# Kernel optimization log

Measured on AMD Instinct MI355X. Metric: run time of the kernel, lower is better.

## Reference

```python
import jax, jax.numpy as jnp
import numpy as np
import math

NUM_CLASSES = 80
CENTER_RADIUS = 2.5
EPS = 1e-7
IMG = 1280.0


def _ciou(gt, pd):
    # gt: [G,4] xyxy, pd: [A,4] xyxy -> CIoU [G,A] (matches ultralytics bbox_iou, CIoU=True)
    b1 = gt[:, None, :]
    b2 = pd[None, :, :]
    iw = jnp.clip(jnp.minimum(b1[..., 2], b2[..., 2]) - jnp.maximum(b1[..., 0], b2[..., 0]), 0.0)
    ih = jnp.clip(jnp.minimum(b1[..., 3], b2[..., 3]) - jnp.maximum(b1[..., 1], b2[..., 1]), 0.0)
    inter = iw * ih
    w1 = b1[..., 2] - b1[..., 0]; h1 = b1[..., 3] - b1[..., 1]
    w2 = b2[..., 2] - b2[..., 0]; h2 = b2[..., 3] - b2[..., 1]
    union = w1 * h1 + w2 * h2 - inter + EPS
    iou = inter / union
    cw = jnp.maximum(b1[..., 2], b2[..., 2]) - jnp.minimum(b1[..., 0], b2[..., 0])
    ch = jnp.maximum(b1[..., 3], b2[..., 3]) - jnp.minimum(b1[..., 1], b2[..., 1])
    c2 = cw * cw + ch * ch + EPS
    rho2 = ((b2[..., 0] + b2[..., 2] - b1[..., 0] - b1[..., 2]) ** 2 +
            (b2[..., 1] + b2[..., 3] - b1[..., 1] - b1[..., 3]) ** 2) / 4.0
    v = (4.0 / math.pi ** 2) * (jnp.arctan(w2 / (h2 + EPS)) - jnp.arctan(w1 / (h1 + EPS))) ** 2
    alpha = v / (v - iou + (1.0 + EPS))
    return iou - (rho2 / c2 + v * alpha)


def _assign_one(scores, boxes, gt_lab, gt_box, valid, stride, anc):
    # scores [A,C], boxes [A,4], gt_lab [G], gt_box [G,4], valid [G] bool, stride [A,1], anc [A,2]
    G = gt_lab.shape[0]
    C = scores.shape[-1]
    # geometry constraint: anchor center within radius*stride of gt center
    gcx = (gt_box[:, 0] + gt_box[:, 2]) / 2.0
    gcy = (gt_box[:, 1] + gt_box[:, 3]) / 2.0
    cd = (stride[:, 0] * CENTER_RADIUS)[None, :]            # [1,A]
    in_center = (jnp.abs(anc[None, :, 0] - gcx[:, None]) < cd) & \
                (jnp.abs(anc[None, :, 1] - gcy[:, None]) < cd)
    in_center = in_center & valid[:, None]                  # [G,A]
    anchor_filter = in_center.any(axis=0)                   # [A]
    # pairwise CIoU (zeroed outside the filtered anchor set / invalid gts)
    ious = jnp.clip(_ciou(gt_box, boxes), 0.0)
    ious = ious * anchor_filter[None, :].astype(ious.dtype) * valid[:, None].astype(ious.dtype)
    iou_loss = -jnp.log(ious + 1e-8)
    # BCE(sqrt(p), onehot) summed over classes, computed without [G,A,C] tensor:
    # sum_c BCE = -sum_c log(1-p_c) - log p_{c_g} + log(1-p_{c_g})
    p = jnp.sqrt(scores)
    logp = jnp.clip(jnp.log(p), -100.0)
    log1mp = jnp.clip(jnp.log1p(-p), -100.0)
    base = -log1mp.sum(-1)                                  # [A]
    lp_g = jnp.take(logp, gt_lab, axis=1).T                 # [G,A]
    l1m_g = jnp.take(log1mp, gt_lab, axis=1).T              # [G,A]
    cls_loss = base[None, :] - lp_g + l1m_g
    # cost; extra 1e8/1e9 penalties emulate torch's exclusion of unfiltered anchors / invalid gts
    cost = (cls_loss + 3.0 * iou_loss
            + 1e6 * (~in_center).astype(cls_loss.dtype)
            + 1e8 * (~anchor_filter)[None, :].astype(cls_loss.dtype)
            + 1e9 * (~valid)[:, None].astype(cls_loss.dtype))
    # dynamic-k: sum of top-10 ious per gt
    topk_ious = jax.lax.top_k(ious, 10)[0]
    dyn_k = jnp.maximum((topk_ious.sum(-1) + 0.5).astype(jnp.int32), 1)
    # per-gt pick dyn_k lowest-cost anchors via rank
    ranks = jnp.argsort(jnp.argsort(cost, axis=-1), axis=-1)
    matching = (ranks < dyn_k[:, None]) & valid[:, None]    # [G,A] bool
    # conflict resolution: anchors matched to >1 gt keep min-cost gt
    cnt = matching.sum(0)                                   # [A]
    best_g = jnp.argmin(cost, axis=0)                       # [A]
    onehot_g = jnp.arange(G)[:, None] == best_g[None, :]
    matching = jnp.where(cnt[None, :] > 1, onehot_g, matching)
    fg = matching.any(axis=0)                               # [A]
    mg = jnp.argmax(matching, axis=0)                       # [A]
    pred_iou = (matching.astype(ious.dtype) * ious).sum(0)  # [A]
    labels = jnp.where(fg, gt_lab[mg], NUM_CLASSES).astype(jnp.int32)
    tboxes = gt_box[mg] * fg[:, None].astype(gt_box.dtype)
    tscores = jax.nn.one_hot(gt_lab[mg], C, dtype=scores.dtype) * (pred_iou * fg)[:, None]
    tgt_idx = jnp.where(fg, mg, 0).astype(jnp.int32)
    return labels, tboxes, tscores, fg, tgt_idx


def setup_inputs() -> dict:
    key = jax.random.key(0)
    ks = jax.random.split(key, 10)
    bs, A, G, C = 16, 33600, 64, NUM_CLASSES
    pd_scores = jax.random.uniform(ks[0], (bs, A, C), jnp.float32, 1e-4, 0.99)
    cxy = jax.random.uniform(ks[1], (bs, A, 2), jnp.float32, 0.0, IMG)
    wh = jax.random.uniform(ks[2], (bs, A, 2), jnp.float32, 8.0, 128.0)
    pd_bboxes = jnp.concatenate([cxy - wh / 2, cxy + wh / 2], axis=-1)
    anc_points = jax.random.uniform(ks[3], (A, 2), jnp.float32, 0.0, IMG)
    gt_labels = jax.random.randint(ks[4], (bs, G, 1), 0, C, jnp.int32)
    gcxy = jax.random.uniform(ks[5], (bs, G, 2), jnp.float32, 64.0, IMG - 64.0)
    gwh = jax.random.uniform(ks[6], (bs, G, 2), jnp.float32, 16.0, 256.0)
    gt_bboxes = jnp.concatenate([gcxy - gwh / 2, gcxy + gwh / 2], axis=-1)
    mask_gt = (jax.random.randint(ks[7], (bs, G, 1), 0, 5, jnp.int32) < 4).astype(jnp.int32)
    stride = (8.0 * (2.0 ** jax.random.randint(ks[8], (bs, A, 1), 0, 3, jnp.int32).astype(jnp.float32)))
    return {"pd_scores": pd_scores, "pd_bboxes": pd_bboxes, "anc_points": anc_points,
            "gt_labels": gt_labels, "gt_bboxes": gt_bboxes, "mask_gt": mask_gt, "stride": stride}


def reference(pd_scores, pd_bboxes, anc_points, gt_labels, gt_bboxes, mask_gt, stride):
    gt_lab = gt_labels[..., 0].astype(jnp.int32)
    valid = mask_gt[..., 0].astype(bool)
    fn = jax.vmap(_assign_one, in_axes=(0, 0, 0, 0, 0, 0, None))
    return fn(pd_scores, pd_bboxes, gt_lab, gt_bboxes, valid, stride, anc_points)
```

## Files before the change

### kernel.cpp

```cpp
#include <hip/hip_runtime.h>
#include <float.h>
#include <math.h>

#define NA 33600
#define NG 64
#define NC 80
#define NB 16
#define CRAD 2.5f
#define MCAP 12288

typedef float vfloat4 __attribute__((ext_vector_type(4)));

#define O_CNT   0ULL
#define O_AG    2150400ULL
#define O_AIOU  4300800ULL
#define O_BASE  6451200ULL
#define O_CCNT  8601600ULL
#define O_CONFC 8601664ULL
#define O_CONFL 8601728ULL
#define O_CA    8667264ULL
#define O_CBASE 9453696ULL
#define O_COLT  10240128ULL
#define WS_NEED_COLT (10240128ULL + 62914560ULL)
#define O_CPB   73154688ULL
#define O_CAP   76300416ULL
#define WS_NEED_PC (76300416ULL + 3145728ULL)
#define O_PIOU  79446144ULL
#define O_PCST  79528064ULL
#define O_PIDX  79609984ULL
#define O_PCI   79691904ULL
#define WS_NEED_SPLIT 79773824ULL

#define OFF_LAB 0L
#define OFF_TB  537600L
#define OFF_TS  2688000L
#define OFF_FG  45696000L
#define OFF_TGT 46233600L
#define OUT_TOTAL 46771200L

__device__ __forceinline__ float ciou_clip(float gx1, float gy1, float gx2, float gy2,
                                           float w1, float h1, float at1, float at2v,
                                           float4 pb) {
    float iw = fmaxf(fminf(gx2, pb.z) - fmaxf(gx1, pb.x), 0.f);
    float ih = fmaxf(fminf(gy2, pb.w) - fmaxf(gy1, pb.y), 0.f);
    float inter = iw * ih;
    float w2 = pb.z - pb.x, h2 = pb.w - pb.y;
    float uni = w1 * h1 + w2 * h2 - inter + 1e-7f;
    float iou = inter / uni;
    float cw = fmaxf(gx2, pb.z) - fminf(gx1, pb.x);
    float ch = fmaxf(gy2, pb.w) - fminf(gy1, pb.y);
    float c2 = cw * cw + ch * ch + 1e-7f;
    float dx = pb.x + pb.z - gx1 - gx2;
    float dy = pb.y + pb.w - gy1 - gy2;
    float rho2 = (dx * dx + dy * dy) * 0.25f;
    float dat = at2v - at1;
    float v = 0.4052847345693511f * (dat * dat);
    float alpha = v / ((v - iou) + 1.0000001f);
    float ci = iou - (rho2 / c2 + v * alpha);
    return fmaxf(ci, 0.f);
}

__global__ __launch_bounds__(256) void k1a_cand(
    const float* __restrict__ anc, const float* __restrict__ gbox,
    const int* __restrict__ gmask, const float* __restrict__ strd,
    int* __restrict__ candA, int* __restrict__ candCnt, int* __restrict__ cnt)
{
    __shared__ float s_gcx[NG], s_gcy[NG];
    __shared__ int s_val[NG];
    const int b = blockIdx.y, tid = threadIdx.x;
    if (tid < NG) {
        const float4 gb = ((const float4*)gbox)[b * NG + tid];
        s_gcx[tid] = (gb.x + gb.z) * 0.5f;
        s_gcy[tid] = (gb.y + gb.w) * 0.5f;
        s_val[tid] = gmask[b * NG + tid];
    }
    __syncthreads();
    const int a = blockIdx.x * 256 + tid;
    int f = 0;
    if (a < NA) {
        cnt[(long)b * NA + a] = 0;
        float2 ap = ((const float2*)anc)[a];
        float cd = strd[(long)b * NA + a] * CRAD;
        for (int g = 0; g < NG; ++g)
            if (s_val[g] && fabsf(ap.x - s_gcx[g]) < cd && fabsf(ap.y - s_gcy[g]) < cd) { f = 1; break; }
    }
    unsigned long long m = __ballot(f);
    int lane = tid & 63;
    int wcnt = __popcll(m);
    int pre = __popcll(m & ((1ULL << lane) - 1ULL));
    int base0 = 0;
    if (lane == 0 && wcnt) base0 = atomicAdd(&candCnt[b], wcnt);
    base0 = __shfl(base0, 0, 64);
    if (f) {
        int pos = base0 + pre;
        if (pos < MCAP) candA[b * MCAP + pos] = a;
    }
}

__global__ __launch_bounds__(256) void k1b_gather(
    const float* __restrict__ scores, const float* __restrict__ pdb,
    const float* __restrict__ anc, const float* __restrict__ strd,
    const int* __restrict__ candCnt, const int* __restrict__ candA,
    float* __restrict__ base, float* __restrict__ candBase,
    float* __restrict__ colT, int use_colT,
    float4* __restrict__ candPB, float4* __restrict__ candAp, int use_pc)
{
    __shared__ float s_l1m[64][81];
    const int b = blockIdx.y;
    int M = candCnt[b]; if (M > MCAP) M = MCAP;
    if (blockIdx.x * 64 >= M) return;
    const int q   = threadIdx.x >> 2;
    const int sub = threadIdx.x & 3;
    const int j = blockIdx.x * 64 + q;
    const bool active = (j < M);
    int a = 0;
    if (active) a = candA[b * MCAP + j];
    const long ia = (long)b * NA + a;
    if (active) {
        if (sub == 1 && use_pc) {
            float4 pb = ((const float4*)pdb)[ia];
            float2 ap = ((const float2*)anc)[a];
            float cd = strd[ia] * CRAD;
            float at2v = atanf((pb.z - pb.x) / ((pb.w - pb.y) + 1e-7f));
            candPB[b * MCAP + j] = pb;
            candAp[b * MCAP + j] = make_float4(ap.x, ap.y, cd, at2v);
        }
        const vfloat4* srow = (const vfloat4*)(scores + ia * NC);
        float* ct = colT + (long)b * NC * MCAP + j;
        #pragma unroll
        for (int qq = 0; qq < 5; ++qq) {
            vfloat4 s4 = __builtin_nontemporal_load(&srow[sub * 5 + qq]);
            float sv[4] = {s4.x, s4.y, s4.z, s4.w};
            #pragma unroll
            for (int k = 0; k < 4; ++k) {
                const int c = sub * 20 + 4 * qq + k;
                float p = sqrtf(sv[k]);
                float l1m = fmaxf(log1pf(-p), -100.f);
                s_l1m[q][c] = l1m;
                if (use_colT) {
                    float lp = fmaxf(logf(p), -100.f);
                    __builtin_nontemporal_store(l1m - lp, &ct[(long)c * MCAP]);
                }
            }
        }
    }
    __syncthreads();
    if (active && sub == 0) {
        float bsum = 0.f;
        #pragma unroll
        for (int c = 0; c < NC; ++c)
            bsum += s_l1m[q][c];
        const float bval = -bsum;
        base[ia] = bval;
        candBase[b * MCAP + j] = bval;
    }
}

__global__ __launch_bounds__(256) void k2_scan(
    const int* __restrict__ glab, const float* __restrict__ gbox,
    const int* __restrict__ gmask,
    const int* __restrict__ candCnt, const int* __restrict__ candA,
    const float* __restrict__ candBase, const float* __restrict__ colT,
    const float4* __restrict__ candPB, const float4* __restrict__ candAp,
    float* __restrict__ partIou, float* __restrict__ partCost,
    int* __restrict__ partIdx, float* __restrict__ partCi)
{
    const int i = blockIdx.y;
    const int s = blockIdx.x;
    const int b = (i & 7) | ((i >> 9) << 3);
    const int g = (i >> 3) & 63;
    if (gmask[b * NG + g] == 0) return;
    const int tid = threadIdx.x, lane = tid & 63, wid = tid >> 6;
    __shared__ float s_v[4];
    __shared__ int s_i[4];

    const float4 gb = ((const float4*)gbox)[b * NG + g];
    const int lab = glab[b * NG + g];
    const float gcx = (gb.x + gb.z) * 0.5f, gcy = (gb.y + gb.w) * 0.5f;
    const float w1 = gb.z - gb.x, h1 = gb.w - gb.y;
    const float at1 = atanf(w1 / (h1 + 1e-7f));
    const int bM = b * MCAP;
    int M = candCnt[b]; if (M > MCAP) M = MCAP;
    const float* colrow = colT + (long)(b * NC + lab) * MCAP;

    float liou[10]; int liodx[10];
    float lcost[10]; int lidx[10]; float lci[10];
    #pragma unroll
    for (int j = 0; j < 10; ++j) {
        liou[j] = 0.f;  liodx[j] = 0x40000000 + tid * 10 + j;
        lcost[j] = FLT_MAX; lidx[j] = 0x40000000 + tid * 10 + j; lci[j] = 0.f;
    }

    for (int jj = s * 256 + tid; jj < M; jj += 512) {
        const int a = candA[bM + jj];
        float4 pb = candPB[bM + jj];
        float4 t  = candAp[bM + jj];
        float ci = ciou_clip(gb.x, gb.y, gb.z, gb.w, w1, h1, at1, t.w, pb);
        bool inc = (fabsf(t.x - gcx) < t.z) && (fabsf(t.y - gcy) < t.z);
        float colv = candBase[bM + jj] + colrow[jj];
        float cost = colv + 3.0f * (-logf(ci + 1e-8f));
        if (!inc) cost += 1e6f;

        if (ci > 0.f && (ci > liou[9] || (ci == liou[9] && a < liodx[9]))) {
            int p10 = 0;
            #pragma unroll
            for (int k = 0; k < 10; ++k)
                p10 += (liou[k] > ci || (liou[k] == ci && liodx[k] < a)) ? 1 : 0;
            #pragma unroll
            for (int j = 9; j >= 0; --j) {
                float pv = (j > 0) ? liou[j - 1] : 0.f;
                int pvi  = (j > 0) ? liodx[j - 1] : 0;
                bool sh = (j > p10), he = (j == p10);
                liou[j]  = sh ? pv  : (he ? ci : liou[j]);
                liodx[j] = sh ? pvi : (he ? a  : liodx[j]);
            }
        }
        if (cost < lcost[9] || (cost == lcost[9] && a < lidx[9])) {
            int p10 = 0;
            #pragma unroll
            for (int k = 0; k < 10; ++k)
                p10 += (lcost[k] < cost || (lcost[k] == cost && lidx[k] < a)) ? 1 : 0;
            #pragma unroll
            for (int j = 9; j >= 0; --j) {
                float pv = (j > 0) ? lcost[j - 1] : FLT_MAX;
                int pvi  = (j > 0) ? lidx[j - 1] : 0;
                float pvc = (j > 0) ? lci[j - 1] : 0.f;
                bool sh = (j > p10), he = (j == p10);
                lcost[j] = sh ? pv  : (he ? cost : lcost[j]);
                lidx[j]  = sh ? pvi : (he ? a    : lidx[j]);
                lci[j]   = sh ? pvc : (he ? ci   : lci[j]);
            }
        }
    }

    const int pbase = i * 20 + s * 10;
    for (int it = 0; it < 10; ++it) {
        float bv = -2.f; int bi = 0x7fffffff;
        #pragma unroll
        for (int j = 0; j < 10; ++j)
            if (liou[j] > bv || (liou[j] == bv && liodx[j] < bi)) { bv = liou[j]; bi = liodx[j]; }
        for (int off = 32; off > 0; off >>= 1) {
            float ov = __shfl_down(bv, off, 64);
            int   oi = __shfl_down(bi, off, 64);
            if (ov > bv || (ov == bv && oi < bi)) { bv = ov; bi = oi; }
        }
        if (lane == 0) { s_v[wid] = bv; s_i[wid] = bi; }
        __syncthreads();
        float wv = s_v[0]; int wi = s_i[0];
        #pragma unroll
        for (int w = 1; w < 4; ++w)
            if (s_v[w] > wv || (s_v[w] == wv && s_i[w] < wi)) { wv = s_v[w]; wi = s_i[w]; }
        if (tid == 0) partIou[pbase + it] = wv;
        #pragma unroll
        for (int j = 0; j < 10; ++j)
            if (liou[j] == wv && liodx[j] == wi) { liou[j] = -2.f; liodx[j] = 0x7fffffff; }
        __syncthreads();
    }
    for (int it = 0; it < 10; ++it) {
        float bc = FLT_MAX; int bi = 0x7fffffff;
        #pragma unroll
        for (int j = 0; j < 10; ++j)
            if (lcost[j] < bc || (lcost[j] == bc && lidx[j] < bi)) { bc = lcost[j]; bi = lidx[j]; }
        for (int off = 32; off > 0; off >>= 1) {
            float oc = __shfl_down(bc, off, 64);
            int   oi = __shfl_down(bi, off, 64);
            if (oc < bc || (oc == bc && oi < bi)) { bc = oc; bi = oi; }
        }
        if (lane == 0) { s_v[wid] = bc; s_i[wid] = bi; }
        __syncthreads();
        float wc = s_v[0]; int wi = s_i[0];
        #pragma unroll
        for (int w = 1; w < 4; ++w)
            if (s_v[w] < wc || (s_v[w] == wc && s_i[w] < wi)) { wc = s_v[w]; wi = s_i[w]; }
        #pragma unroll
        for (int j = 0; j < 10; ++j)
            if (lcost[j] == wc && lidx[j] == wi) {
                partCost[pbase + it] = wc;
                partIdx[pbase + it]  = wi;
                partCi[pbase + it]   = lci[j];
                lcost[j] = FLT_MAX; lidx[j] = 0x7fffffff;
            }
        __syncthreads();
    }
}

__global__ __launch_bounds__(256) void k2b_merge(
    const int* __restrict__ gmask,
    const float* __restrict__ partIou, const float* __restrict__ partCost,
    const int* __restrict__ partIdx, const float* __restrict__ partCi,
    int* __restrict__ cnt, int* __restrict__ ag, float* __restrict__ aiou)
{
    const int lane = threadIdx.x & 63;
    const int wv0 = blockIdx.x * 4 + (threadIdx.x >> 6);
    for (int i = wv0; i < NB * NG; i += gridDim.x * 4) {
        const int b = (i & 7) | ((i >> 9) << 3);
        const int g = (i >> 3) & 63;
        if (gmask[b * NG + g] == 0) continue;
        float v = (lane < 20) ? partIou[i * 20 + lane] : -2.f;
        float acc = 0.f;
        for (int it = 0; it < 10; ++it) {
            float bv = v;
            for (int off = 32; off > 0; off >>= 1) {
                float ov = __shfl_down(bv, off, 64);
                if (ov > bv) bv = ov;
            }
            bv = __shfl(bv, 0, 64);
            acc += bv;
            unsigned long long m = __ballot(v == bv);
            int first = (int)(__ffsll((long long)m)) - 1;
            if (lane == first) v = -3.f;
        }
        int K = (int)(acc + 0.5f);
        if (K < 1) K = 1;

        float c  = (lane < 20) ? partCost[i * 20 + lane] : FLT_MAX;
        int  idx = (lane < 20) ? partIdx[i * 20 + lane] : 0x7fffffff;
        float ci = (lane < 20) ? partCi[i * 20 + lane] : 0.f;
        const long bA = (long)b * NA;
        for (int it = 0; it < K; ++it) {
            float bc = c; int bi = idx;
            for (int off = 32; off > 0; off >>= 1) {
                float oc = __shfl_down(bc, off, 64);
                int   oi = __shfl_down(bi, off, 64);
                if (oc < bc || (oc == bc && oi < bi)) { bc = oc; bi = oi; }
            }
            bc = __shfl(bc, 0, 64); bi = __shfl(bi, 0, 64);
            const bool own = (c == bc && idx == bi);
            if (own && bi < NA) {
                atomicAdd(&cnt[bA + bi], 1);
                ag[bA + bi] = g;
                aiou[bA + bi] = ci;
            }
            if (own) { c = FLT_MAX; idx = 0x7fffffff; }
        }
    }
}

__global__ __launch_bounds__(256) void k2_select(
    const float* __restrict__ scores, const float* __restrict__ pdb,
    const float* __restrict__ anc, const int* __restrict__ glab,
    const float* __restrict__ gbox, const int* __restrict__ gmask,
    const float* __restrict__ strd,
    const int* __restrict__ candCnt, const int* __restrict__ candA,
    const float* __restrict__ candBase, const float* __restrict__ colT, int use_colT,
    const float4* __restrict__ candPB, const float4* __restrict__ candAp, int use_pc,
    int* __restrict__ cnt, int* __restrict__ ag, float* __restrict__ aiou)
{
    const int i = blockIdx.x;
    const int b = (i & 7) | ((i >> 9) << 3);
    const int g = (i >> 3) & 63;
    if (gmask[b * NG + g] == 0) return;
    const int tid = threadIdx.x, lane = tid & 63, wid = tid >> 6;
    __shared__ float s_v[4];
    __shared__ int s_i[4];

    const float4 gb = ((const float4*)gbox)[b * NG + g];
    const int lab = glab[b * NG + g];
    const float gcx = (gb.x + gb.z) * 0.5f, gcy = (gb.y + gb.w) * 0.5f;
    const float w1 = gb.z - gb.x, h1 = gb.w - gb.y;
    const float at1 = atanf(w1 / (h1 + 1e-7f));
    const long bA = (long)b * NA;
    const int bM = b * MCAP;
    int M = candCnt[b]; if (M > MCAP) M = MCAP;
    const float* colrow = colT + (long)(b * NC + lab) * MCAP;

    float liou[10]; int liodx[10];
    float lcost[10]; int lidx[10]; float lci[10];
    #pragma unroll
    for (int j = 0; j < 10; ++j) {
        liou[j] = 0.f;  liodx[j] = 0x40000000 + tid * 10 + j;
        lcost[j] = FLT_MAX; lidx[j] = 0x40000000 + tid * 10 + j; lci[j] = 0.f;
    }

    for (int jj = tid; jj < M; jj += 256) {
        const int a = candA[bM + jj];
        const long ia = bA + a;
        float4 pb; float apx, apy, cd, at2v;
        if (use_pc) {
            pb = candPB[bM + jj];
            float4 t = candAp[bM + jj];
            apx = t.x; apy = t.y; cd = t.z; at2v = t.w;
        } else {
            pb = ((const float4*)pdb)[ia];
            at2v = atanf((pb.z - pb.x) / ((pb.w - pb.y) + 1e-7f));
            float2 ap = ((const float2*)anc)[a];
            apx = ap.x; apy = ap.y;
            cd = strd[ia] * CRAD;
        }
        float ci = ciou_clip(gb.x, gb.y, gb.z, gb.w, w1, h1, at1, at2v, pb);
        bool inc = (fabsf(apx - gcx) < cd) && (fabsf(apy - gcy) < cd);
        float colv;
        if (use_colT) {
            colv = candBase[bM + jj] + colrow[jj];
        } else {
            float s = scores[ia * (long)NC + lab];
            float p = sqrtf(s);
            colv = candBase[bM + jj] + (fmaxf(log1pf(-p), -100.f) - fmaxf(logf(p), -100.f));
        }
        float cost = colv + 3.0f * (-logf(ci + 1e-8f));
        if (!inc) cost += 1e6f;

        if (ci > 0.f && (ci > liou[9] || (ci == liou[9] && a < liodx[9]))) {
            int p10 = 0;
            #pragma unroll
            for (int k = 0; k < 10; ++k)
                p10 += (liou[k] > ci || (liou[k] == ci && liodx[k] < a)) ? 1 : 0;
            #pragma unroll
            for (int j = 9; j >= 0; --j) {
                float pv = (j > 0) ? liou[j - 1] : 0.f;
                int pvi  = (j > 0) ? liodx[j - 1] : 0;
                bool sh = (j > p10), he = (j == p10);
                liou[j]  = sh ? pv  : (he ? ci : liou[j]);
                liodx[j] = sh ? pvi : (he ? a  : liodx[j]);
            }
        }
        if (cost < lcost[9] || (cost == lcost[9] && a < lidx[9])) {
            int p10 = 0;
            #pragma unroll
            for (int k = 0; k < 10; ++k)
                p10 += (lcost[k] < cost || (lcost[k] == cost && lidx[k] < a)) ? 1 : 0;
            #pragma unroll
            for (int j = 9; j >= 0; --j) {
                float pv = (j > 0) ? lcost[j - 1] : FLT_MAX;
                int pvi  = (j > 0) ? lidx[j - 1] : 0;
                float pvc = (j > 0) ? lci[j - 1] : 0.f;
                bool sh = (j > p10), he = (j == p10);
                lcost[j] = sh ? pv  : (he ? cost : lcost[j]);
                lidx[j]  = sh ? pvi : (he ? a    : lidx[j]);
                lci[j]   = sh ? pvc : (he ? ci   : lci[j]);
            }
        }
    }

    float acc = 0.f;
    for (int it = 0; it < 10; ++it) {
        float bv = -2.f; int bi = 0x7fffffff;
        #pragma unroll
        for (int j = 0; j < 10; ++j)
            if (liou[j] > bv || (liou[j] == bv && liodx[j] < bi)) { bv = liou[j]; bi = liodx[j]; }
        for (int off = 32; off > 0; off >>= 1) {
            float ov = __shfl_down(bv, off, 64);
            int   oi = __shfl_down(bi, off, 64);
            if (ov > bv || (ov == bv && oi < bi)) { bv = ov; bi = oi; }
        }
        if (lane == 0) { s_v[wid] = bv; s_i[wid] = bi; }
        __syncthreads();
        float wv = s_v[0]; int wi = s_i[0];
        #pragma unroll
        for (int w = 1; w < 4; ++w)
            if (s_v[w] > wv || (s_v[w] == wv && s_i[w] < wi)) { wv = s_v[w]; wi = s_i[w]; }
        acc += wv;
        #pragma unroll
        for (int j = 0; j < 10; ++j)
            if (liou[j] == wv && liodx[j] == wi) { liou[j] = -2.f; liodx[j] = 0x7fffffff; }
        __syncthreads();
    }
    int K = (int)(acc + 0.5f);
    if (K < 1) K = 1;

    for (int it = 0; it < K; ++it) {
        float bc = FLT_MAX; int bi = 0x7fffffff;
        #pragma unroll
        for (int j = 0; j < 10; ++j)
            if (lcost[j] < bc || (lcost[j] == bc && lidx[j] < bi)) { bc = lcost[j]; bi = lidx[j]; }
        for (int off = 32; off > 0; off >>= 1) {
            float oc = __shfl_down(bc, off, 64);
            int   oi = __shfl_down(bi, off, 64);
            if (oc < bc || (oc == bc && oi < bi)) { bc = oc; bi = oi; }
        }
        if (lane == 0) { s_v[wid] = bc; s_i[wid] = bi; }
        __syncthreads();
        float wc = s_v[0]; int wi = s_i[0];
        #pragma unroll
        for (int w = 1; w < 4; ++w)
            if (s_v[w] < wc || (s_v[w] == wc && s_i[w] < wi)) { wc = s_v[w]; wi = s_i[w]; }
        if (wi < NA) {
            #pragma unroll
            for (int j = 0; j < 10; ++j)
                if (lcost[j] == wc && lidx[j] == wi) {
                    atomicAdd(&cnt[bA + wi], 1);
                    ag[bA + wi] = g;
                    aiou[bA + wi] = lci[j];
                    lcost[j] = FLT_MAX; lidx[j] = 0x7fffffff;
                }
        }
        __syncthreads();
    }
}

__global__ __launch_bounds__(256) void k3_main(
    const int* __restrict__ glab, const float* __restrict__ gbox,
    const int* __restrict__ cnt, const int* __restrict__ ag, const float* __restrict__ aiou,
    int* __restrict__ confCnt, int* __restrict__ confList, float* __restrict__ out)
{
    const int tid = threadIdx.x;
    const long i = (long)blockIdx.x * 256 + tid;
    const int b = (int)(i / NA);
    const int c = cnt[i];
    float labo = 80.f;
    const bool conflict = (c > 1);
    if (c == 1) {
        int g = ag[i]; float iou = aiou[i];
        int lb = glab[b * NG + g];
        labo = (float)lb;
        ((float4*)(out + OFF_TB))[i] = ((const float4*)gbox)[b * NG + g];
        out[OFF_FG + i] = 1.f;
        out[OFF_TGT + i] = (float)g;
        out[OFF_TS + i * NC + lb] = iou;
    }
    unsigned long long m = __ballot(conflict ? 1 : 0);
    int lane = tid & 63;
    int wcnt = __popcll(m);
    int pre = __popcll(m & ((1ULL << lane) - 1ULL));
    int base0 = 0;
    if (lane == 0 && wcnt) base0 = atomicAdd(confCnt, wcnt);
    base0 = __shfl(base0, 0, 64);
    if (conflict) confList[base0 + pre] = (int)i;
    else out[OFF_LAB + i] = labo;
}

__global__ __launch_bounds__(256) void k3b_conflict(
    const float* __restrict__ scores, const float* __restrict__ pdb,
    const float* __restrict__ anc, const int* __restrict__ glab,
    const float* __restrict__ gbox, const int* __restrict__ gmask,
    const float* __restrict__ strd, const float* __restrict__ base,
    const int* __restrict__ confCnt, const int* __restrict__ confList,
    float* __restrict__ out)
{
    const int lane = threadIdx.x & 63;
    const int waveId = blockIdx.x * 4 + (threadIdx.x >> 6);
    const int nWaves = gridDim.x * 4;
    int n = *confCnt; if (n > 16384) n = 16384;
    for (int idx = waveId; idx < n; idx += nWaves) {
        const long i = (long)confList[idx];
        const int b = (int)(i / NA); const int a = (int)(i % NA);
        const int g = lane;
        float4 pb = ((const float4*)pdb)[i];
        float bse = base[i];
        float at2v = atanf((pb.z - pb.x) / ((pb.w - pb.y) + 1e-7f));
        float2 ap = ((const float2*)anc)[a];
        float cd = strd[i] * CRAD;
        float cost = FLT_MAX; float iom = 0.f;
        if (gmask[b * NG + g] != 0) {
            float4 gb = ((const float4*)gbox)[b * NG + g];
            float w1 = gb.z - gb.x, h1 = gb.w - gb.y;
            float at1 = atanf(w1 / (h1 + 1e-7f));
            iom = ciou_clip(gb.x, gb.y, gb.z, gb.w, w1, h1, at1, at2v, pb);
            float gcx = (gb.x + gb.z) * 0.5f, gcy = (gb.y + gb.w) * 0.5f;
            bool inc = (fabsf(ap.x - gcx) < cd) && (fabsf(ap.y - gcy) < cd);
            int lb = glab[b * NG + g];
            float s = scores[i * (long)NC + lb];
            float p = sqrtf(s);
            float clsv = bse + (fmaxf(log1pf(-p), -100.f) - fmaxf(logf(p), -100.f));
            cost = clsv + 3.0f * (-logf(iom + 1e-8f));
            if (!inc) cost += 1e6f;
        }
        float bc = cost; int bg = g; float bio = iom;
        for (int off = 32; off > 0; off >>= 1) {
            float oc = __shfl_down(bc, off, 64);
            int   og = __shfl_down(bg, off, 64);
            float oo = __shfl_down(bio, off, 64);
            if (oc < bc || (oc == bc && og < bg)) { bc = oc; bg = og; bio = oo; }
        }
        if (lane == 0) {
            int lb = glab[b * NG + bg];
            out[OFF_LAB + i] = (float)lb;
            ((float4*)(out + OFF_TB))[i] = ((const float4*)gbox)[b * NG + bg];
            out[OFF_FG + i] = 1.f;
            out[OFF_TGT + i] = (float)bg;
            out[OFF_TS + i * NC + lb] = bio;
        }
    }
}

extern "C" void kernel_launch(void* const* d_in, const int* in_sizes, int n_in,
                              void* d_out, int out_size, void* d_ws, size_t ws_size,
                              hipStream_t stream) {
    const float* scores = (const float*)d_in[0];
    const float* pdb    = (const float*)d_in[1];
    const float* anc    = (const float*)d_in[2];
    const int*   glab   = (const int*)d_in[3];
    const float* gbox   = (const float*)d_in[4];
    const int*   gmask  = (const int*)d_in[5];
    const float* strd   = (const float*)d_in[6];
    float* out = (float*)d_out;
    char* ws = (char*)d_ws;

    int*    cnt      = (int*)(ws + O_CNT);
    int*    ag       = (int*)(ws + O_AG);
    float*  aiou     = (float*)(ws + O_AIOU);
    float*  base     = (float*)(ws + O_BASE);
    int*    candCnt  = (int*)(ws + O_CCNT);
    int*    confCnt  = (int*)(ws + O_CONFC);
    int*    confList = (int*)(ws + O_CONFL);
    int*    candA    = (int*)(ws + O_CA);
    float*  candBase = (float*)(ws + O_CBASE);
    float*  colT     = (float*)(ws + O_COLT);
    float4* candPB   = (float4*)(ws + O_CPB);
    float4* candAp   = (float4*)(ws + O_CAP);
    float*  partIou  = (float*)(ws + O_PIOU);
    float*  partCost = (float*)(ws + O_PCST);
    int*    partIdx  = (int*)(ws + O_PIDX);
    float*  partCi   = (float*)(ws + O_PCI);
    const int use_colT  = (ws_size >= WS_NEED_COLT) ? 1 : 0;
    const int use_pc    = (ws_size >= WS_NEED_PC) ? 1 : 0;
    const int use_split = (ws_size >= WS_NEED_SPLIT) ? 1 : 0;

    (void)hipMemsetAsync(out + OFF_TB, 0, (size_t)(OUT_TOTAL - OFF_TB) * sizeof(float), stream);
    (void)hipMemsetAsync(candCnt, 0, 128, stream);
    k1a_cand<<<dim3((NA + 255) / 256, NB), 256, 0, stream>>>(
        anc, gbox, gmask, strd, candA, candCnt, cnt);
    k1b_gather<<<dim3((MCAP + 63) / 64, NB), 256, 0, stream>>>(
        scores, pdb, anc, strd, candCnt, candA, base, candBase, colT, use_colT,
        candPB, candAp, use_pc);
    if (use_split) {
        k2_scan<<<dim3(2, NB * NG), 256, 0, stream>>>(
            glab, gbox, gmask, candCnt, candA, candBase, colT, candPB, candAp,
            partIou, partCost, partIdx, partCi);
        k2b_merge<<<64, 256, 0, stream>>>(
            gmask, partIou, partCost, partIdx, partCi, cnt, ag, aiou);
    } else {
        k2_select<<<NB * NG, 256, 0, stream>>>(
            scores, pdb, anc, glab, gbox, gmask, strd,
            candCnt, candA, candBase, colT, use_colT, candPB, candAp, use_pc,
            cnt, ag, aiou);
    }
    k3_main<<<(NB * NA) / 256, 256, 0, stream>>>(
        glab, gbox, cnt, ag, aiou, confCnt, confList, out);
    k3b_conflict<<<128, 256, 0, stream>>>(
        scores, pdb, anc, glab, gbox, gmask, strd, base,
        confCnt, confList, out);
}
```

Baseline: 626.2 us.

## Pack anchor index and slot into one key, simplify per-thread top-k in scan

Candidate anchors now get a packed 32-bit key (anchor index high, candidate slot low), written in k1a. The scan kernel keeps sorted top-10 lists with a cheaper insertion step and drops the per-entry CIoU and index arrays. Extraction pops only the list heads, and the IoU reduction uses fmaxf plus a ballot. The merge kernel recomputes CIoU for the few selected anchors from the slot stored in the key. This cuts register pressure and compare work in the hot scan loop, at the cost of an extra key array and a dependence on anchor indices fitting in 16 bits.

```diff
diff --git a/kernel.cpp b/kernel.cpp
--- a/kernel.cpp
+++ b/kernel.cpp
@@ -28,8 +28,8 @@
 #define O_PIOU  79446144ULL
 #define O_PCST  79528064ULL
 #define O_PIDX  79609984ULL
-#define O_PCI   79691904ULL
-#define WS_NEED_SPLIT 79773824ULL
+#define O_CKEY  79773824ULL
+#define WS_NEED_KEY (79773824ULL + 786432ULL)
 
 #define OFF_LAB 0L
 #define OFF_TB  537600L
@@ -63,7 +63,8 @@
 __global__ __launch_bounds__(256) void k1a_cand(
     const float* __restrict__ anc, const float* __restrict__ gbox,
     const int* __restrict__ gmask, const float* __restrict__ strd,
-    int* __restrict__ candA, int* __restrict__ candCnt, int* __restrict__ cnt)
+    int* __restrict__ candA, unsigned int* __restrict__ candKey, int use_key,
+    int* __restrict__ candCnt, int* __restrict__ cnt)
 {
     __shared__ float s_gcx[NG], s_gcy[NG];
     __shared__ int s_val[NG];
@@ -93,7 +94,10 @@
     base0 = __shfl(base0, 0, 64);
     if (f) {
         int pos = base0 + pre;
-        if (pos < MCAP) candA[b * MCAP + pos] = a;
+        if (pos < MCAP) {
+            candA[b * MCAP + pos] = a;
+            if (use_key) candKey[b * MCAP + pos] = ((unsigned int)a << 16) | (unsigned int)pos;
+        }
     }
 }
 
@@ -159,11 +163,11 @@
 __global__ __launch_bounds__(256) void k2_scan(
     const int* __restrict__ glab, const float* __restrict__ gbox,
     const int* __restrict__ gmask,
-    const int* __restrict__ candCnt, const int* __restrict__ candA,
+    const int* __restrict__ candCnt, const unsigned int* __restrict__ candKey,
     const float* __restrict__ candBase, const float* __restrict__ colT,
     const float4* __restrict__ candPB, const float4* __restrict__ candAp,
     float* __restrict__ partIou, float* __restrict__ partCost,
-    int* __restrict__ partIdx, float* __restrict__ partCi)
+    unsigned int* __restrict__ partIdx)
 {
     const int i = blockIdx.y;
     const int s = blockIdx.x;
@@ -173,6 +177,7 @@
     const int tid = threadIdx.x, lane = tid & 63, wid = tid >> 6;
     __shared__ float s_v[4];
     __shared__ int s_i[4];
+    __shared__ unsigned int s_u[4];
 
     const float4 gb = ((const float4*)gbox)[b * NG + g];
     const int lab = glab[b * NG + g];
@@ -183,111 +188,105 @@
     int M = candCnt[b]; if (M > MCAP) M = MCAP;
     const float* colrow = colT + (long)(b * NC + lab) * MCAP;
 
-    float liou[10]; int liodx[10];
-    float lcost[10]; int lidx[10]; float lci[10];
+    float liou[10];
+    float lcost[10]; unsigned int lkey[10];
     #pragma unroll
     for (int j = 0; j < 10; ++j) {
-        liou[j] = 0.f;  liodx[j] = 0x40000000 + tid * 10 + j;
-        lcost[j] = FLT_MAX; lidx[j] = 0x40000000 + tid * 10 + j; lci[j] = 0.f;
+        liou[j] = 0.f;
+        lcost[j] = FLT_MAX; lkey[j] = 0xFFFFFFFFu;
     }
 
     for (int jj = s * 256 + tid; jj < M; jj += 512) {
-        const int a = candA[bM + jj];
-        float4 pb = candPB[bM + jj];
-        float4 t  = candAp[bM + jj];
+        const unsigned int key = candKey[bM + jj];
+        const float4 pb = candPB[bM + jj];
+        const float4 t  = candAp[bM + jj];
+        const float cb  = candBase[bM + jj];
+        const float cr  = colrow[jj];
         float ci = ciou_clip(gb.x, gb.y, gb.z, gb.w, w1, h1, at1, t.w, pb);
         bool inc = (fabsf(t.x - gcx) < t.z) && (fabsf(t.y - gcy) < t.z);
-        float colv = candBase[bM + jj] + colrow[jj];
+        float colv = cb + cr;
         float cost = colv + 3.0f * (-logf(ci + 1e-8f));
         if (!inc) cost += 1e6f;
 
-        if (ci > 0.f && (ci > liou[9] || (ci == liou[9] && a < liodx[9]))) {
-            int p10 = 0;
-            #pragma unroll
-            for (int k = 0; k < 10; ++k)
-                p10 += (liou[k] > ci || (liou[k] == ci && liodx[k] < a)) ? 1 : 0;
-            #pragma unroll
-            for (int j = 9; j >= 0; --j) {
-                float pv = (j > 0) ? liou[j - 1] : 0.f;
-                int pvi  = (j > 0) ? liodx[j - 1] : 0;
-                bool sh = (j > p10), he = (j == p10);
-                liou[j]  = sh ? pv  : (he ? ci : liou[j]);
-                liodx[j] = sh ? pvi : (he ? a  : liodx[j]);
+        if (ci > liou[9]) {
+            #pragma unroll
+            for (int k = 9; k >= 1; --k) {
+                bool ck   = (liou[k] > ci);
+                bool ckm1 = (liou[k - 1] > ci);
+                liou[k] = ck ? liou[k] : (ckm1 ? ci : liou[k - 1]);
             }
-        }
-        if (cost < lcost[9] || (cost == lcost[9] && a < lidx[9])) {
-            int p10 = 0;
-            #pragma unroll
-            for (int k = 0; k < 10; ++k)
-                p10 += (lcost[k] < cost || (lcost[k] == cost && lidx[k] < a)) ? 1 : 0;
-            #pragma unroll
-            for (int j = 9; j >= 0; --j) {
-                float pv = (j > 0) ? lcost[j - 1] : FLT_MAX;
-                int pvi  = (j > 0) ? lidx[j - 1] : 0;
-                float pvc = (j > 0) ? lci[j - 1] : 0.f;
-                bool sh = (j > p10), he = (j == p10);
-                lcost[j] = sh ? pv  : (he ? cost : lcost[j]);
-                lidx[j]  = sh ? pvi : (he ? a    : lidx[j]);
-                lci[j]   = sh ? pvc : (he ? ci   : lci[j]);
+            liou[0] = (liou[0] > ci) ? liou[0] : ci;
+        }
+        if (cost < lcost[9] || (cost == lcost[9] && key < lkey[9])) {
+            #pragma unroll
+            for (int k = 9; k >= 1; --k) {
+                bool ck   = (lcost[k] < cost) || (lcost[k] == cost && lkey[k] < key);
+                bool ckm1 = (lcost[k - 1] < cost) || (lcost[k - 1] == cost && lkey[k - 1] < key);
+                lcost[k] = ck ? lcost[k] : (ckm1 ? cost : lcost[k - 1]);
+                lkey[k]  = ck ? lkey[k]  : (ckm1 ? key  : lkey[k - 1]);
             }
+            bool c0 = (lcost[0] < cost) || (lcost[0] == cost && lkey[0] < key);
+            lcost[0] = c0 ? lcost[0] : cost;
+            lkey[0]  = c0 ? lkey[0]  : key;
         }
     }
 
     const int pbase = i * 20 + s * 10;
     for (int it = 0; it < 10; ++it) {
-        float bv = -2.f; int bi = 0x7fffffff;
-        #pragma unroll
-        for (int j = 0; j < 10; ++j)
-            if (liou[j] > bv || (liou[j] == bv && liodx[j] < bi)) { bv = liou[j]; bi = liodx[j]; }
-        for (int off = 32; off > 0; off >>= 1) {
-            float ov = __shfl_down(bv, off, 64);
-            int   oi = __shfl_down(bi, off, 64);
-            if (ov > bv || (ov == bv && oi < bi)) { bv = ov; bi = oi; }
-        }
-        if (lane == 0) { s_v[wid] = bv; s_i[wid] = bi; }
-        __syncthreads();
-        float wv = s_v[0]; int wi = s_i[0];
-        #pragma unroll
-        for (int w = 1; w < 4; ++w)
-            if (s_v[w] > wv || (s_v[w] == wv && s_i[w] < wi)) { wv = s_v[w]; wi = s_i[w]; }
+        float bv = liou[0];
+        #pragma unroll
+        for (int off = 32; off > 0; off >>= 1)
+            bv = fmaxf(bv, __shfl_down(bv, off, 64));
+        if (lane == 0) s_v[wid] = bv;
+        __syncthreads();
+        float wv = fmaxf(fmaxf(s_v[0], s_v[1]), fmaxf(s_v[2], s_v[3]));
         if (tid == 0) partIou[pbase + it] = wv;
-        #pragma unroll
-        for (int j = 0; j < 10; ++j)
-            if (liou[j] == wv && liodx[j] == wi) { liou[j] = -2.f; liodx[j] = 0x7fffffff; }
+        unsigned long long m = __ballot(liou[0] == wv);
+        int fl = m ? (int)__ffsll((long long)m) - 1 : 64;
+        if (lane == 0) s_i[wid] = fl;
+        __syncthreads();
+        int ow, ol;
+        if (s_i[0] < 64)      { ow = 0; ol = s_i[0]; }
+        else if (s_i[1] < 64) { ow = 1; ol = s_i[1]; }
+        else if (s_i[2] < 64) { ow = 2; ol = s_i[2]; }
+        else                  { ow = 3; ol = s_i[3]; }
+        if (wid == ow && lane == ol) {
+            #pragma unroll
+            for (int k = 0; k < 9; ++k) liou[k] = liou[k + 1];
+            liou[9] = -2.f;
+        }
         __syncthreads();
     }
     for (int it = 0; it < 10; ++it) {
-        float bc = FLT_MAX; int bi = 0x7fffffff;
-        #pragma unroll
-        for (int j = 0; j < 10; ++j)
-            if (lcost[j] < bc || (lcost[j] == bc && lidx[j] < bi)) { bc = lcost[j]; bi = lidx[j]; }
+        float bc = lcost[0]; unsigned int bk = lkey[0];
+        #pragma unroll
         for (int off = 32; off > 0; off >>= 1) {
             float oc = __shfl_down(bc, off, 64);
-            int   oi = __shfl_down(bi, off, 64);
-            if (oc < bc || (oc == bc && oi < bi)) { bc = oc; bi = oi; }
-        }
-        if (lane == 0) { s_v[wid] = bc; s_i[wid] = bi; }
-        __syncthreads();
-        float wc = s_v[0]; int wi = s_i[0];
+            unsigned int ok = __shfl_down(bk, off, 64);
+            if (oc < bc || (oc == bc && ok < bk)) { bc = oc; bk = ok; }
+        }
+        if (lane == 0) { s_v[wid] = bc; s_u[wid] = bk; }
+        __syncthreads();
+        float wc = s_v[0]; unsigned int wk = s_u[0];
         #pragma unroll
         for (int w = 1; w < 4; ++w)
-            if (s_v[w] < wc || (s_v[w] == wc && s_i[w] < wi)) { wc = s_v[w]; wi = s_i[w]; }
-        #pragma unroll
-        for (int j = 0; j < 10; ++j)
-            if (lcost[j] == wc && lidx[j] == wi) {
-                partCost[pbase + it] = wc;
-                partIdx[pbase + it]  = wi;
-                partCi[pbase + it]   = lci[j];
-                lcost[j] = FLT_MAX; lidx[j] = 0x7fffffff;
-            }
+            if (s_v[w] < wc || (s_v[w] == wc && s_u[w] < wk)) { wc = s_v[w]; wk = s_u[w]; }
+        if (lcost[0] == wc && lkey[0] == wk) {
+            partCost[pbase + it] = wc;
+            partIdx[pbase + it]  = wk;
+            #pragma unroll
+            for (int k = 0; k < 9; ++k) { lcost[k] = lcost[k + 1]; lkey[k] = lkey[k + 1]; }
+            lcost[9] = FLT_MAX; lkey[9] = 0xFFFFFFFFu;
+        }
         __syncthreads();
     }
 }
 
 __global__ __launch_bounds__(256) void k2b_merge(
-    const int* __restrict__ gmask,
+    const int* __restrict__ gmask, const float* __restrict__ gbox,
     const float* __restrict__ partIou, const float* __restrict__ partCost,
-    const int* __restrict__ partIdx, const float* __restrict__ partCi,
+    const unsigned int* __restrict__ partIdx,
+    const float4* __restrict__ candPB, const float4* __restrict__ candAp,
     int* __restrict__ cnt, int* __restrict__ ag, float* __restrict__ aiou)
 {
     const int lane = threadIdx.x & 63;
@@ -300,38 +299,51 @@
         float acc = 0.f;
         for (int it = 0; it < 10; ++it) {
             float bv = v;
-            for (int off = 32; off > 0; off >>= 1) {
-                float ov = __shfl_down(bv, off, 64);
-                if (ov > bv) bv = ov;
-            }
+            #pragma unroll
+            for (int off = 32; off > 0; off >>= 1)
+                bv = fmaxf(bv, __shfl_down(bv, off, 64));
             bv = __shfl(bv, 0, 64);
             acc += bv;
             unsigned long long m = __ballot(v == bv);
-            int first = (int)(__ffsll((long long)m)) - 1;
+            int first = (int)__ffsll((long long)m) - 1;
             if (lane == first) v = -3.f;
         }
         int K = (int)(acc + 0.5f);
         if (K < 1) K = 1;
 
+        const float4 gbw = ((const float4*)gbox)[b * NG + g];
+        const float w1w = gbw.z - gbw.x, h1w = gbw.w - gbw.y;
+        const float at1w = atanf(w1w / (h1w + 1e-7f));
+        const long bA = (long)b * NA;
+        const int bM = b * MCAP;
         float c  = (lane < 20) ? partCost[i * 20 + lane] : FLT_MAX;
-        int  idx = (lane < 20) ? partIdx[i * 20 + lane] : 0x7fffffff;
-        float ci = (lane < 20) ? partCi[i * 20 + lane] : 0.f;
-        const long bA = (long)b * NA;
+        unsigned int idx = (lane < 20) ? partIdx[i * 20 + lane] : 0xFFFFFFFFu;
         for (int it = 0; it < K; ++it) {
-            float bc = c; int bi = idx;
+            float bc = c; unsigned int bk = idx;
+            #pragma unroll
             for (int off = 32; off > 0; off >>= 1) {
                 float oc = __shfl_down(bc, off, 64);
-                int   oi = __shfl_down(bi, off, 64);
-                if (oc < bc || (oc == bc && oi < bi)) { bc = oc; bi = oi; }
+                unsigned int ok = __shfl_down(bk, off, 64);
+                if (oc < bc || (oc == bc && ok < bk)) { bc = oc; bk = ok; }
             }
-            bc = __shfl(bc, 0, 64); bi = __shfl(bi, 0, 64);
-            const bool own = (c == bc && idx == bi);
-            if (own && bi < NA) {
-                atomicAdd(&cnt[bA + bi], 1);
-                ag[bA + bi] = g;
-                aiou[bA + bi] = ci;
+            bc = __shfl(bc, 0, 64);
+            bk = (unsigned int)__shfl((int)bk, 0, 64);
+            bool own = (c == bc && idx == bk);
+            unsigned long long mo = __ballot(own);
+            int fl = (int)__ffsll((long long)mo) - 1;
+            if (own && lane == fl) {
+                unsigned int aa = bk >> 16;
+                if (aa < NA) {
+                    int j = (int)(bk & 0xFFFFu);
+                    float4 pbw = candPB[bM + j];
+                    float4 tw  = candAp[bM + j];
+                    float ciw = ciou_clip(gbw.x, gbw.y, gbw.z, gbw.w, w1w, h1w, at1w, tw.w, pbw);
+                    atomicAdd(&cnt[bA + aa], 1);
+                    ag[bA + aa] = g;
+                    aiou[bA + aa] = ciw;
+                }
             }
-            if (own) { c = FLT_MAX; idx = 0x7fffffff; }
+            if (own) { c = FLT_MAX; idx = 0xFFFFFFFFu; }
         }
     }
 }
@@ -600,25 +612,25 @@
     float4* candAp   = (float4*)(ws + O_CAP);
     float*  partIou  = (float*)(ws + O_PIOU);
     float*  partCost = (float*)(ws + O_PCST);
-    int*    partIdx  = (int*)(ws + O_PIDX);
-    float*  partCi   = (float*)(ws + O_PCI);
+    unsigned int* partIdx = (unsigned int*)(ws + O_PIDX);
+    unsigned int* candKey = (unsigned int*)(ws + O_CKEY);
     const int use_colT  = (ws_size >= WS_NEED_COLT) ? 1 : 0;
     const int use_pc    = (ws_size >= WS_NEED_PC) ? 1 : 0;
-    const int use_split = (ws_size >= WS_NEED_SPLIT) ? 1 : 0;
+    const int use_split = (ws_size >= WS_NEED_KEY && use_colT && use_pc) ? 1 : 0;
 
     (void)hipMemsetAsync(out + OFF_TB, 0, (size_t)(OUT_TOTAL - OFF_TB) * sizeof(float), stream);
     (void)hipMemsetAsync(candCnt, 0, 128, stream);
     k1a_cand<<<dim3((NA + 255) / 256, NB), 256, 0, stream>>>(
-        anc, gbox, gmask, strd, candA, candCnt, cnt);
+        anc, gbox, gmask, strd, candA, candKey, use_split, candCnt, cnt);
     k1b_gather<<<dim3((MCAP + 63) / 64, NB), 256, 0, stream>>>(
         scores, pdb, anc, strd, candCnt, candA, base, candBase, colT, use_colT,
         candPB, candAp, use_pc);
     if (use_split) {
         k2_scan<<<dim3(2, NB * NG), 256, 0, stream>>>(
-            glab, gbox, gmask, candCnt, candA, candBase, colT, candPB, candAp,
-            partIou, partCost, partIdx, partCi);
+            glab, gbox, gmask, candCnt, candKey, candBase, colT, candPB, candAp,
+            partIou, partCost, partIdx);
         k2b_merge<<<64, 256, 0, stream>>>(
-            gmask, partIou, partCost, partIdx, partCi, cnt, ag, aiou);
+            gmask, gbox, partIou, partCost, partIdx, candPB, candAp, cnt, ag, aiou);
     } else {
         k2_select<<<NB * NG, 256, 0, stream>>>(
             scores, pdb, anc, glab, gbox, gmask, strd,
```

Result: faster. 584.9 us (-6.6%).
